# Optimization experiments

Hardware: AMD Instinct MI355X
Metric: run time of the kernel (lower is better)

The kernel has to match this reference:

```python
import jax, jax.numpy as jnp
import numpy as np
import math

CH, CTX, NH, G = 512, 768, 8, 32
EPS = 1e-5

def setup_inputs() -> dict:
    key = jax.random.key(0)
    ks = jax.random.split(key, 12)
    s = 0.02
    return {
        "x": jax.random.normal(ks[0], (1, CH, 64, 64), dtype=jnp.float32),
        "context": jax.random.normal(ks[1], (1, CTX, 64, 64), dtype=jnp.float32),
        "gn_w": jnp.ones((CH,), jnp.float32),
        "gn_b": jnp.zeros((CH,), jnp.float32),
        "wq": jax.random.normal(ks[2], (CH, CH), jnp.float32) * s,
        "bq": jnp.zeros((CH,), jnp.float32),
        "wk": jax.random.normal(ks[3], (CH, CTX), jnp.float32) * s,
        "bk": jnp.zeros((CH,), jnp.float32),
        "wv": jax.random.normal(ks[4], (CH, CTX), jnp.float32) * s,
        "bv": jnp.zeros((CH,), jnp.float32),
        "wo": jax.random.normal(ks[5], (CH, CH), jnp.float32) * s,
        "bo": jnp.zeros((CH,), jnp.float32),
    }

def _group_norm(x, w, b):
    B, C, H, W = x.shape
    r = x.reshape(B, G, C // G, H, W)
    mu = jnp.mean(r, axis=(2, 3, 4), keepdims=True)
    var = jnp.var(r, axis=(2, 3, 4), keepdims=True)
    r = (r - mu) * jax.lax.rsqrt(var + EPS)
    return r.reshape(B, C, H, W) * w[None, :, None, None] + b[None, :, None, None]

def _conv1x1(x, w, b):
    # x: [B,Cin,H,W], w: [Cout,Cin]
    return jnp.einsum('bchw,oc->bohw', x, w) + b[None, :, None, None]

def reference(x, context, gn_w, gn_b, wq, bq, wk, bk, wv, bv, wo, bo):
    B, C, H, W = x.shape
    residual = x
    h = _group_norm(x, gn_w, gn_b)
    q = _conv1x1(h, wq, bq).reshape(B, NH, C // NH, H * W)
    k = _conv1x1(context, wk, bk).reshape(B, NH, C // NH, H * W)
    v = _conv1x1(context, wv, bv).reshape(B, NH, C // NH, H * W)
    scale = 1.0 / math.sqrt(C // NH)
    # chunked softmax in the original is mathematically exact full softmax
    attn = jnp.einsum('bhdi,bhdj->bhij', q, k) * scale
    attn = jax.nn.softmax(attn, axis=-1)
    out = jnp.einsum('bhij,bhdj->bhdi', attn, v).reshape(B, C, H, W)
    out = _conv1x1(out, wo, bo)
    return out + residual
```

## Files before the change

kernel.cpp:

```cpp
#include <hip/hip_runtime.h>
#include <cstdint>
#include <cstddef>

typedef __attribute__((ext_vector_type(8))) short bf16x8;
typedef __attribute__((ext_vector_type(4))) float f32x4;
typedef unsigned short u16;

#define QSCALE (0.125f * 1.44269504088896f)

__device__ inline u16 f2bf(float x) {
  uint32_t u = __builtin_bit_cast(uint32_t, x);
  u += 0x7FFFu + ((u >> 16) & 1u);
  return (u16)(u >> 16);
}
__device__ inline float bf2f(u16 v) {
  return __builtin_bit_cast(float, (uint32_t)v << 16);
}
__device__ inline uint32_t cvtpk(float a, float b) {
  uint32_t r;
  asm("v_cvt_pk_bf16_f32 %0, %1, %2" : "=v"(r) : "v"(a), "v"(b));
  return r;
}
__device__ inline float exp2raw(float x) {
  float r;
  asm("v_exp_f32 %0, %1" : "=v"(r) : "v"(x));
  return r;
}
__device__ inline void gload_lds16(const void* g, void* l) {
  __builtin_amdgcn_global_load_lds(
      (const __attribute__((address_space(1))) char*)g,
      (__attribute__((address_space(3))) char*)l, 16, 0, 0);
}

__global__ __launch_bounds__(256) void gn_partial(const float* __restrict__ x,
                                                  float* __restrict__ gpart,
                                                  float* __restrict__ gpart2) {
  __shared__ float rs[4], rss[4];
  int b = blockIdx.x;
  int g = b >> 3, sl = b & 7;
  const float* base = x + (size_t)g * 65536 + sl * 8192;
  int t = threadIdx.x;
  float s = 0.f, ss = 0.f;
#pragma unroll
  for (int i = 0; i < 8; ++i) {
    float4 v = *reinterpret_cast<const float4*>(base + i * 1024 + t * 4);
    s += v.x + v.y + v.z + v.w;
    ss += v.x * v.x + v.y * v.y + v.z * v.z + v.w * v.w;
  }
  for (int d = 32; d; d >>= 1) {
    s += __shfl_down(s, d, 64);
    ss += __shfl_down(ss, d, 64);
  }
  int wid = t >> 6;
  if ((t & 63) == 0) { rs[wid] = s; rss[wid] = ss; }
  __syncthreads();
  if (t == 0) {
    gpart[b] = rs[0] + rs[1] + rs[2] + rs[3];
    gpart2[b] = rss[0] + rss[1] + rss[2] + rss[3];
  }
}

__global__ __launch_bounds__(256) void prep(const float* __restrict__ wq, u16* __restrict__ wqB,
                                            const float* __restrict__ wk, u16* __restrict__ wkB,
                                            const float* __restrict__ wv, u16* __restrict__ wvB,
                                            const float* __restrict__ wo, u16* __restrict__ woB,
                                            const float* __restrict__ x, u16* __restrict__ hT,
                                            const float* __restrict__ ctx, u16* __restrict__ ctxT,
                                            const float* __restrict__ gnw, const float* __restrict__ gnb,
                                            const float* __restrict__ gpart, const float* __restrict__ gpart2) {
  int b = blockIdx.x;
  int t = threadIdx.x;
  if (b < 1280) {
    const float* s; u16* d; int off;
    if (b < 256)       { s = wq; d = wqB; off = b; }
    else if (b < 640)  { s = wk; d = wkB; off = b - 256; }
    else if (b < 1024) { s = wv; d = wvB; off = b - 640; }
    else               { s = wo; d = woB; off = b - 1024; }
    int i = (off * 256 + t) * 4;
    float4 v = *reinterpret_cast<const float4*>(s + i);
    u16 o[4] = {f2bf(v.x), f2bf(v.y), f2bf(v.z), f2bf(v.w)};
    *reinterpret_cast<uint2*>(d + i) = *reinterpret_cast<const uint2*>(o);
    return;
  }
  __shared__ float tile[64][65];
  __shared__ float smu[4], srs[4];
  const float* in; u16* out; int C, p0, c0;
  bool norm = false;
  if (b < 1792) {
    int idx = b - 1280;
    in = x; out = hT; C = 512; p0 = (idx & 63) * 64; c0 = (idx >> 6) * 64; norm = true;
  } else {
    int idx = b - 1792;
    in = ctx; out = ctxT; C = 768; p0 = (idx & 63) * 64; c0 = (idx >> 6) * 64;
  }
  if (norm) {
    if (t < 4) {
      int g = (c0 >> 4) + t;
      float S = 0.f, SS = 0.f;
#pragma unroll
      for (int sIdx = 0; sIdx < 8; ++sIdx) {
        S += gpart[g * 8 + sIdx];
        SS += gpart2[g * 8 + sIdx];
      }
      float mu = S * (1.f / 65536.f);
      float var = SS * (1.f / 65536.f) - mu * mu;
      smu[t] = mu;
      srs[t] = rsqrtf(var + 1e-5f);
    }
    __syncthreads();
  }
  int cl = t >> 4, pl = (t & 15) * 4;
#pragma unroll
  for (int rep = 0; rep < 4; ++rep) {
    int c = cl + rep * 16;
    float4 v = *reinterpret_cast<const float4*>(in + (size_t)(c0 + c) * 4096 + p0 + pl);
    float s = 1.f, f = 0.f;
    if (norm) {
      s = gnw[c0 + c] * srs[rep];
      f = gnb[c0 + c] - smu[rep] * s;
    }
    tile[c][pl + 0] = v.x * s + f;
    tile[c][pl + 1] = v.y * s + f;
    tile[c][pl + 2] = v.z * s + f;
    tile[c][pl + 3] = v.w * s + f;
  }
  __syncthreads();
#pragma unroll
  for (int rep = 0; rep < 16; ++rep) {
    int idx = rep * 256 + t;
    int pw = idx >> 6, cw = idx & 63;
    out[(size_t)(p0 + pw) * C + c0 + cw] = f2bf(tile[cw][pw]);
  }
}

template <int BIAS_MODE>
__device__ inline void gemm_body(u16* __restrict__ aT, u16* __restrict__ bT,
                                 const u16* __restrict__ A, const u16* __restrict__ B,
                                 u16* __restrict__ Dv,
                                 const float* __restrict__ bias,
                                 int Rb, int K, float oscale, int bx, int by) {
  const int t = threadIdx.x;
  const int lane = t & 63, w = t >> 6;
  const int wr = w >> 1, wc = w & 1;
  const int l15 = lane & 15, l4 = lane >> 4;
  const int i0 = by * 128, j0 = bx * 64;
  const int r_st = t >> 3, slot = t & 7;
  f32x4 acc[4][2] = {};

  auto stage = [&](int kt, int b) {
#pragma unroll
    for (int q = 0; q < 4; ++q) {
      int row = q * 32 + r_st;
      int koff = kt + ((slot ^ (row & 7)) * 8);
      gload_lds16(A + (size_t)(i0 + row) * K + koff, (char*)aT + b * 16384 + q * 4096 + w * 1024);
    }
#pragma unroll
    for (int q = 0; q < 2; ++q) {
      int row = q * 32 + r_st;
      int koff = kt + ((slot ^ (row & 7)) * 8);
      gload_lds16(B + (size_t)(j0 + row) * K + koff, (char*)bT + b * 8192 + q * 4096 + w * 1024);
    }
  };

  const int nt = K / 64;
  stage(0, 0);
  stage(64, 1);

  for (int tt = 0; tt < nt; ++tt) {
    const int cur = tt % 3;
    if (tt + 1 < nt) asm volatile("s_waitcnt vmcnt(6)\n\ts_barrier" ::: "memory");
    else             asm volatile("s_waitcnt vmcnt(0)\n\ts_barrier" ::: "memory");
    if (tt + 2 < nt) stage((tt + 2) * 64, (tt + 2) % 3);

#pragma unroll
    for (int kk = 0; kk < 2; ++kk) {
      bf16x8 af[4], bfr[2];
#pragma unroll
      for (int m = 0; m < 4; ++m) {
        int row = wr * 64 + m * 16 + l15;
        int off = row * 128 + ((l4 * 16 + kk * 64) ^ ((row & 7) << 4));
        af[m] = *reinterpret_cast<const bf16x8*>((const char*)aT + cur * 16384 + off);
      }
#pragma unroll
      for (int n = 0; n < 2; ++n) {
        int row = wc * 32 + n * 16 + l15;
        int off = row * 128 + ((l4 * 16 + kk * 64) ^ ((row & 7) << 4));
        bfr[n] = *reinterpret_cast<const bf16x8*>((const char*)bT + cur * 8192 + off);
      }
#pragma unroll
      for (int m = 0; m < 4; ++m)
#pragma unroll
        for (int n = 0; n < 2; ++n)
          acc[m][n] = __builtin_amdgcn_mfma_f32_16x16x32_bf16(af[m], bfr[n], acc[m][n], 0, 0, 0);
    }
  }

#pragma unroll
  for (int m = 0; m < 4; ++m) {
    int ib = i0 + wr * 64 + m * 16 + l4 * 4;
#pragma unroll
    for (int n = 0; n < 2; ++n) {
      int j = j0 + wc * 32 + n * 16 + l15;
#pragma unroll
      for (int r = 0; r < 4; ++r) {
        int i = ib + r;
        float v = acc[m][n][r];
        if (BIAS_MODE == 0) v += bias[i];
        else v += bias[j];
        v *= oscale;
        Dv[(size_t)i * Rb + j] = f2bf(v);
      }
    }
  }
}

__global__ __launch_bounds__(256) void gemm_all(const u16* __restrict__ hT, const u16* __restrict__ ctxT,
                                                const u16* __restrict__ wqB, const u16* __restrict__ wkB,
                                                const u16* __restrict__ wvB,
                                                u16* __restrict__ QT, u16* __restrict__ KT, u16* __restrict__ Vb,
                                                const float* __restrict__ bq, const float* __restrict__ bk,
                                                const float* __restrict__ bv) {
  __shared__ u16 aT[3][128 * 64];
  __shared__ u16 bT[3][64 * 64];
  int b = blockIdx.x;
  if (b < 256)
    gemm_body<1>(&aT[0][0], &bT[0][0], hT, wqB, QT, bq, 512, 512, QSCALE, b & 7, b >> 3);
  else if (b < 512)
    gemm_body<1>(&aT[0][0], &bT[0][0], ctxT, wkB, KT, bk, 512, 768, 1.0f, (b - 256) & 7, (b - 256) >> 3);
  else
    gemm_body<0>(&aT[0][0], &bT[0][0], wvB, ctxT, Vb, bv, 4096, 768, 1.0f, (b - 512) & 63, (b - 512) >> 6);
}

__global__ __launch_bounds__(256) void gemm_projF(const u16* __restrict__ woB,
                                                  const u16* __restrict__ P0, const u16* __restrict__ P1,
                                                  const u16* __restrict__ P2, const u16* __restrict__ P3,
                                                  const float* __restrict__ Lb,
                                                  float* __restrict__ D, const float* __restrict__ bo,
                                                  const float* __restrict__ res) {
  __shared__ u16 aT[3][128 * 64];
  __shared__ u16 bT[2][64 * 64];
  __shared__ float sinv[512];
  const int t = threadIdx.x;
  const int lane = t & 63, w = t >> 6;
  const int wr = w >> 1, wc = w & 1;
  const int l15 = lane & 15, l4 = lane >> 4;
  const int bx = blockIdx.x & 63, by = blockIdx.x >> 6;
  const int i0 = by * 128, j0 = bx * 64;
  const int r_st = t >> 3, slot = t & 7;

  {
#pragma unroll
    for (int r = 0; r < 2; ++r) {
      int idx = t * 2 + r;
      int hh = idx >> 6, jj = idx & 63;
      int o = hh * 4096 + j0 + jj;
      float den = Lb[o] + Lb[32768 + o] + Lb[65536 + o] + Lb[98304 + o];
      sinv[idx] = 1.f / den;
    }
  }

  auto stageA = [&](int kt, int b) {
#pragma unroll
    for (int q = 0; q < 4; ++q) {
      int row = q * 32 + r_st;
      int koff = kt + ((slot ^ (row & 7)) * 8);
      gload_lds16(woB + (size_t)(i0 + row) * 512 + koff, (char*)aT + b * 16384 + q * 4096 + w * 1024);
    }
  };

  const int brow = t >> 2;
  const int bc0 = (t & 3) * 2;
  uint4 rv[2][4];
  auto loadB = [&](int kt) {
#pragma unroll
    for (int c = 0; c < 2; ++c) {
      size_t off = (size_t)(j0 + brow) * 512 + kt + (bc0 + c) * 8;
      rv[c][0] = *reinterpret_cast<const uint4*>(P0 + off);
      rv[c][1] = *reinterpret_cast<const uint4*>(P1 + off);
      rv[c][2] = *reinterpret_cast<const uint4*>(P2 + off);
      rv[c][3] = *reinterpret_cast<const uint4*>(P3 + off);
    }
  };
  auto writeB = [&](int kt, int buf) {
    float inv = sinv[((kt >> 6) << 6) + brow];
#pragma unroll
    for (int c = 0; c < 2; ++c) {
      uint32_t pk[4];
#pragma unroll
      for (int wi = 0; wi < 4; ++wi) {
        uint32_t w0 = (wi == 0) ? rv[c][0].x : (wi == 1) ? rv[c][0].y : (wi == 2) ? rv[c][0].z : rv[c][0].w;
        uint32_t w1 = (wi == 0) ? rv[c][1].x : (wi == 1) ? rv[c][1].y : (wi == 2) ? rv[c][1].z : rv[c][1].w;
        uint32_t w2 = (wi == 0) ? rv[c][2].x : (wi == 1) ? rv[c][2].y : (wi == 2) ? rv[c][2].z : rv[c][2].w;
        uint32_t w3 = (wi == 0) ? rv[c][3].x : (wi == 1) ? rv[c][3].y : (wi == 2) ? rv[c][3].z : rv[c][3].w;
        float lo = __builtin_bit_cast(float, w0 << 16) + __builtin_bit_cast(float, w1 << 16) +
                   __builtin_bit_cast(float, w2 << 16) + __builtin_bit_cast(float, w3 << 16);
        float hi = __builtin_bit_cast(float, w0 & 0xFFFF0000u) + __builtin_bit_cast(float, w1 & 0xFFFF0000u) +
                   __builtin_bit_cast(float, w2 & 0xFFFF0000u) + __builtin_bit_cast(float, w3 & 0xFFFF0000u);
        pk[wi] = cvtpk(lo * inv, hi * inv);
      }
      uint4 outv = {pk[0], pk[1], pk[2], pk[3]};
      int off = brow * 128 + (((bc0 + c) ^ (brow & 7)) * 16);
      *reinterpret_cast<uint4*>((char*)&bT[buf][0] + off) = outv;
    }
  };

  stageA(0, 0);
  stageA(64, 1);
  loadB(0);
  asm volatile("s_waitcnt vmcnt(4)" ::: "memory");
  writeB(0, 0);
  asm volatile("s_waitcnt lgkmcnt(0)\n\ts_barrier" ::: "memory");

  f32x4 acc[4][2] = {};
  for (int tt = 0; tt < 8; ++tt) {
    const int cur = tt & 1;
    if (tt + 1 < 8) loadB((tt + 1) * 64);

#pragma unroll
    for (int kk = 0; kk < 2; ++kk) {
      bf16x8 af[4], bfr[2];
#pragma unroll
      for (int m = 0; m < 4; ++m) {
        int row = wr * 64 + m * 16 + l15;
        int off = row * 128 + ((l4 * 16 + kk * 64) ^ ((row & 7) << 4));
        af[m] = *reinterpret_cast<const bf16x8*>((const char*)aT + (tt % 3) * 16384 + off);
      }
#pragma unroll
      for (int n = 0; n < 2; ++n) {
        int row = wc * 32 + n * 16 + l15;
        int off = row * 128 + ((l4 * 16 + kk * 64) ^ ((row & 7) << 4));
        bfr[n] = *reinterpret_cast<const bf16x8*>((const char*)&bT[cur][0] + off);
      }
#pragma unroll
      for (int m = 0; m < 4; ++m)
#pragma unroll
        for (int n = 0; n < 2; ++n)
          acc[m][n] = __builtin_amdgcn_mfma_f32_16x16x32_bf16(af[m], bfr[n], acc[m][n], 0, 0, 0);
    }

    if (tt + 2 < 8) stageA((tt + 2) * 64, (tt + 2) % 3);
    if (tt + 1 < 8) {
      if (tt + 2 < 8) asm volatile("s_waitcnt vmcnt(4)" ::: "memory");
      else            asm volatile("s_waitcnt vmcnt(0)" ::: "memory");
      writeB((tt + 1) * 64, cur ^ 1);
    }
    asm volatile("s_waitcnt lgkmcnt(0)\n\ts_barrier" ::: "memory");
  }

#pragma unroll
  for (int m = 0; m < 4; ++m) {
    int ib = i0 + wr * 64 + m * 16 + l4 * 4;
#pragma unroll
    for (int n = 0; n < 2; ++n) {
      int j = j0 + wc * 32 + n * 16 + l15;
#pragma unroll
      for (int r = 0; r < 4; ++r) {
        int i = ib + r;
        float v = acc[m][n][r] + bo[i] + res[(size_t)i * 4096 + j];
        D[(size_t)i * 4096 + j] = v;
      }
    }
  }
}

__global__ __launch_bounds__(256) void attn_kernel(const u16* __restrict__ QT,
                                                   const u16* __restrict__ KT,
                                                   const u16* __restrict__ V,
                                                   u16* __restrict__ P0, u16* __restrict__ P1,
                                                   u16* __restrict__ P2, u16* __restrict__ P3,
                                                   float* __restrict__ Lb) {
  __shared__ u16 kbuf[2][64 * 64];
  __shared__ u16 vbuf[2][64 * 64];
  const int t = threadIdx.x;
  const int lane = t & 63, w = t >> 6;
  const int l15 = lane & 15, l4 = lane >> 4;
  int id = blockIdx.x;
  id = (id & 7) * 128 + (id >> 3);
  const int z = id >> 8;
  const int h = (id >> 5) & 7;
  const int q0 = (id & 31) * 128;
  const int tile0 = z * 16;
  const int r_st = t >> 3, slot = t & 7;

  bf16x8 qa[2][2];
#pragma unroll
  for (int f = 0; f < 2; ++f) {
    int qrow = q0 + w * 32 + f * 16 + l15;
    qa[f][0] = *reinterpret_cast<const bf16x8*>(QT + (size_t)qrow * 512 + h * 64 + l4 * 8);
    qa[f][1] = *reinterpret_cast<const bf16x8*>(QT + (size_t)qrow * 512 + h * 64 + 32 + l4 * 8);
  }

  f32x4 o0[4] = {}, o1[4] = {};
  f32x4 la0 = {}, la1 = {};
  const short oneb = (short)0x3F80;
  const bf16x8 ones = {oneb, oneb, oneb, oneb, oneb, oneb, oneb, oneb};

  int off0[4], off1[4];
#pragma unroll
  for (int n = 0; n < 4; ++n) {
    int row = n * 16 + l15, sw = (row & 7) << 4;
    off0[n] = row * 128 + ((l4 * 16) ^ sw);
    off1[n] = row * 128 + ((l4 * 16 + 64) ^ sw);
  }

  auto stageK = [&](int tile, int b) {
#pragma unroll
    for (int q = 0; q < 2; ++q) {
      int row = q * 32 + r_st;
      int so = (slot ^ (row & 7)) * 8;
      gload_lds16(KT + (size_t)(tile * 64 + row) * 512 + h * 64 + so,
                  (char*)kbuf[b] + q * 4096 + w * 1024);
    }
  };
  auto stageV = [&](int tile, int b) {
#pragma unroll
    for (int q = 0; q < 2; ++q) {
      int row = q * 32 + r_st;
      int so = ((((slot & 1) * 4 + (slot >> 1)) ^ (row & 7)) * 8);
      gload_lds16(V + (size_t)(h * 64 + row) * 4096 + tile * 64 + so,
                  (char*)vbuf[b] + q * 4096 + w * 1024);
    }
  };

  stageK(tile0, 0);
  stageV(tile0, 0);

#pragma unroll 2
  for (int kt = 0; kt < 16; ++kt) {
    const int cur = kt & 1;
    asm volatile("s_waitcnt vmcnt(0)\n\ts_barrier" ::: "memory");
    if (kt + 1 < 16) { stageK(tile0 + kt + 1, cur ^ 1); stageV(tile0 + kt + 1, cur ^ 1); }

    f32x4 s0[4], s1[4];
#pragma unroll
    for (int n = 0; n < 4; ++n) {
      bf16x8 kb0 = *reinterpret_cast<const bf16x8*>((const char*)kbuf[cur] + off0[n]);
      bf16x8 kb1 = *reinterpret_cast<const bf16x8*>((const char*)kbuf[cur] + off1[n]);
      f32x4 za = {};
      za = __builtin_amdgcn_mfma_f32_16x16x32_bf16(kb0, qa[0][0], za, 0, 0, 0);
      za = __builtin_amdgcn_mfma_f32_16x16x32_bf16(kb1, qa[0][1], za, 0, 0, 0);
      s0[n] = za;
      f32x4 zb = {};
      zb = __builtin_amdgcn_mfma_f32_16x16x32_bf16(kb0, qa[1][0], zb, 0, 0, 0);
      zb = __builtin_amdgcn_mfma_f32_16x16x32_bf16(kb1, qa[1][1], zb, 0, 0, 0);
      s1[n] = zb;
    }

#pragma unroll
    for (int n = 0; n < 4; ++n)
#pragma unroll
      for (int r = 0; r < 4; ++r) {
        s0[n][r] = exp2raw(s0[n][r]);
        s1[n][r] = exp2raw(s1[n][r]);
      }

    bf16x8 pa[2][2];
    {
      uint32_t u00 = cvtpk(s0[0][0], s0[0][1]), u01 = cvtpk(s0[0][2], s0[0][3]);
      uint32_t u10 = cvtpk(s0[1][0], s0[1][1]), u11 = cvtpk(s0[1][2], s0[1][3]);
      uint32_t u20 = cvtpk(s0[2][0], s0[2][1]), u21 = cvtpk(s0[2][2], s0[2][3]);
      uint32_t u30 = cvtpk(s0[3][0], s0[3][1]), u31 = cvtpk(s0[3][2], s0[3][3]);
      asm volatile("v_permlane16_swap_b32 %0, %1" : "+v"(u00), "+v"(u20));
      asm volatile("v_permlane16_swap_b32 %0, %1" : "+v"(u01), "+v"(u21));
      asm volatile("v_permlane16_swap_b32 %0, %1" : "+v"(u10), "+v"(u30));
      asm volatile("v_permlane16_swap_b32 %0, %1" : "+v"(u11), "+v"(u31));
      int4 p0i = {(int)u00, (int)u01, (int)u20, (int)u21};
      int4 p1i = {(int)u10, (int)u11, (int)u30, (int)u31};
      pa[0][0] = __builtin_bit_cast(bf16x8, p0i);
      pa[0][1] = __builtin_bit_cast(bf16x8, p1i);
    }
    {
      uint32_t u00 = cvtpk(s1[0][0], s1[0][1]), u01 = cvtpk(s1[0][2], s1[0][3]);
      uint32_t u10 = cvtpk(s1[1][0], s1[1][1]), u11 = cvtpk(s1[1][2], s1[1][3]);
      uint32_t u20 = cvtpk(s1[2][0], s1[2][1]), u21 = cvtpk(s1[2][2], s1[2][3]);
      uint32_t u30 = cvtpk(s1[3][0], s1[3][1]), u31 = cvtpk(s1[3][2], s1[3][3]);
      asm volatile("v_permlane16_swap_b32 %0, %1" : "+v"(u00), "+v"(u20));
      asm volatile("v_permlane16_swap_b32 %0, %1" : "+v"(u01), "+v"(u21));
      asm volatile("v_permlane16_swap_b32 %0, %1" : "+v"(u10), "+v"(u30));
      asm volatile("v_permlane16_swap_b32 %0, %1" : "+v"(u11), "+v"(u31));
      int4 p0i = {(int)u00, (int)u01, (int)u20, (int)u21};
      int4 p1i = {(int)u10, (int)u11, (int)u30, (int)u31};
      pa[1][0] = __builtin_bit_cast(bf16x8, p0i);
      pa[1][1] = __builtin_bit_cast(bf16x8, p1i);
    }

    la0 = __builtin_amdgcn_mfma_f32_16x16x32_bf16(pa[0][0], ones, la0, 0, 0, 0);
    la0 = __builtin_amdgcn_mfma_f32_16x16x32_bf16(pa[0][1], ones, la0, 0, 0, 0);
    la1 = __builtin_amdgcn_mfma_f32_16x16x32_bf16(pa[1][0], ones, la1, 0, 0, 0);
    la1 = __builtin_amdgcn_mfma_f32_16x16x32_bf16(pa[1][1], ones, la1, 0, 0, 0);

#pragma unroll
    for (int dt = 0; dt < 4; ++dt) {
      bf16x8 vb0 = *reinterpret_cast<const bf16x8*>((const char*)vbuf[cur] + off0[dt]);
      bf16x8 vb1 = *reinterpret_cast<const bf16x8*>((const char*)vbuf[cur] + off1[dt]);
      o0[dt] = __builtin_amdgcn_mfma_f32_16x16x32_bf16(pa[0][0], vb0, o0[dt], 0, 0, 0);
      o0[dt] = __builtin_amdgcn_mfma_f32_16x16x32_bf16(pa[0][1], vb1, o0[dt], 0, 0, 0);
      o1[dt] = __builtin_amdgcn_mfma_f32_16x16x32_bf16(pa[1][0], vb0, o1[dt], 0, 0, 0);
      o1[dt] = __builtin_amdgcn_mfma_f32_16x16x32_bf16(pa[1][1], vb1, o1[dt], 0, 0, 0);
    }
  }

  u16* obase = (z == 0) ? P0 : (z == 1) ? P1 : (z == 2) ? P2 : P3;
#pragma unroll
  for (int r = 0; r < 4; ++r) {
    int orow0 = q0 + w * 32 + l4 * 4 + r;
#pragma unroll
    for (int dt = 0; dt < 4; ++dt) {
      obase[(size_t)orow0 * 512 + h * 64 + dt * 16 + l15] = f2bf(o0[dt][r]);
      obase[(size_t)(orow0 + 16) * 512 + h * 64 + dt * 16 + l15] = f2bf(o1[dt][r]);
    }
  }
  if (l15 == 0) {
    int q = q0 + w * 32 + l4 * 4;
#pragma unroll
    for (int r = 0; r < 4; ++r) {
      Lb[z * 32768 + h * 4096 + q + r] = la0[r];
      Lb[z * 32768 + h * 4096 + q + r + 16] = la1[r];
    }
  }
}

extern "C" void kernel_launch(void* const* d_in, const int* in_sizes, int n_in,
                              void* d_out, int out_size, void* d_ws, size_t ws_size,
                              hipStream_t stream) {
  const float* x    = (const float*)d_in[0];
  const float* ctx  = (const float*)d_in[1];
  const float* gn_w = (const float*)d_in[2];
  const float* gn_b = (const float*)d_in[3];
  const float* wq   = (const float*)d_in[4];
  const float* bq   = (const float*)d_in[5];
  const float* wk   = (const float*)d_in[6];
  const float* bk   = (const float*)d_in[7];
  const float* wv   = (const float*)d_in[8];
  const float* bv   = (const float*)d_in[9];
  const float* wo   = (const float*)d_in[10];
  const float* bo   = (const float*)d_in[11];

  char* ws = (char*)d_ws;
  float* gpart  = (float*)ws;
  float* gpart2 = gpart + 256;
  u16* woB    = (u16*)(ws + 4096);
  u16* wqB    = woB + 512 * 512;
  u16* wkB    = wqB + 512 * 512;
  u16* wvB    = wkB + 512 * 768;
  u16* hT     = wvB + 512 * 768;
  u16* ctxT   = hT + 4096 * 512;
  u16* QT     = ctxT + 4096 * 768;
  u16* KT     = QT + 4096 * 512;
  u16* Vb     = KT + 4096 * 512;
  u16* OtT    = Vb + (size_t)512 * 4096;
  float* Lb   = (float*)(OtT + (size_t)4096 * 512);
  u16* P0     = wqB;
  u16* P1     = P0 + (size_t)4096 * 512;
  u16* P2     = P1 + (size_t)4096 * 512;
  u16* P3     = OtT;

  gn_partial<<<256, 256, 0, stream>>>(x, gpart, gpart2);
  prep<<<2560, 256, 0, stream>>>(wq, wqB, wk, wkB, wv, wvB, wo, woB,
                                 x, hT, ctx, ctxT, gn_w, gn_b, gpart, gpart2);

  gemm_all<<<768, 256, 0, stream>>>(hT, ctxT, wqB, wkB, wvB, QT, KT, Vb, bq, bk, bv);

  attn_kernel<<<1024, 256, 0, stream>>>(QT, KT, Vb, P0, P1, P2, P3, Lb);

  gemm_projF<<<256, 256, 0, stream>>>(woB, P0, P1, P2, P3, Lb, (float*)d_out, bo, x);
}
```

Baseline: 96.47 us.

## Regroup prep kernels to overlap stats with casts; double-buffer QKV GEMM

Merges the group-norm partial-statistics pass with the weight casts and the context transpose into one launch. The normalize-and-transpose of x moves into a second kernel, so only that part waits on the statistics and the independent work overlaps with the reduction. Separately, the QKV GEMM goes from triple buffering (two stages of prefetch) to double buffering with a full vmcnt(0) wait each step. That cuts LDS use and may raise occupancy, at the cost of less latency hiding for global loads.

```diff
diff --git a/kernel.cpp b/kernel.cpp
--- a/kernel.cpp
+++ b/kernel.cpp
@@ -32,50 +32,47 @@
       (__attribute__((address_space(3))) char*)l, 16, 0, 0);
 }
 
-__global__ __launch_bounds__(256) void gn_partial(const float* __restrict__ x,
-                                                  float* __restrict__ gpart,
-                                                  float* __restrict__ gpart2) {
-  __shared__ float rs[4], rss[4];
-  int b = blockIdx.x;
-  int g = b >> 3, sl = b & 7;
-  const float* base = x + (size_t)g * 65536 + sl * 8192;
-  int t = threadIdx.x;
-  float s = 0.f, ss = 0.f;
-#pragma unroll
-  for (int i = 0; i < 8; ++i) {
-    float4 v = *reinterpret_cast<const float4*>(base + i * 1024 + t * 4);
-    s += v.x + v.y + v.z + v.w;
-    ss += v.x * v.x + v.y * v.y + v.z * v.z + v.w * v.w;
-  }
-  for (int d = 32; d; d >>= 1) {
-    s += __shfl_down(s, d, 64);
-    ss += __shfl_down(ss, d, 64);
-  }
-  int wid = t >> 6;
-  if ((t & 63) == 0) { rs[wid] = s; rss[wid] = ss; }
-  __syncthreads();
-  if (t == 0) {
-    gpart[b] = rs[0] + rs[1] + rs[2] + rs[3];
-    gpart2[b] = rss[0] + rss[1] + rss[2] + rss[3];
-  }
-}
-
-__global__ __launch_bounds__(256) void prep(const float* __restrict__ wq, u16* __restrict__ wqB,
-                                            const float* __restrict__ wk, u16* __restrict__ wkB,
-                                            const float* __restrict__ wv, u16* __restrict__ wvB,
-                                            const float* __restrict__ wo, u16* __restrict__ woB,
-                                            const float* __restrict__ x, u16* __restrict__ hT,
-                                            const float* __restrict__ ctx, u16* __restrict__ ctxT,
-                                            const float* __restrict__ gnw, const float* __restrict__ gnb,
-                                            const float* __restrict__ gpart, const float* __restrict__ gpart2) {
+__global__ __launch_bounds__(256) void prep_a(const float* __restrict__ x,
+                                              float* __restrict__ gpart,
+                                              float* __restrict__ gpart2,
+                                              const float* __restrict__ wq, u16* __restrict__ wqB,
+                                              const float* __restrict__ wk, u16* __restrict__ wkB,
+                                              const float* __restrict__ wv, u16* __restrict__ wvB,
+                                              const float* __restrict__ wo, u16* __restrict__ woB,
+                                              const float* __restrict__ ctx, u16* __restrict__ ctxT) {
   int b = blockIdx.x;
   int t = threadIdx.x;
-  if (b < 1280) {
-    const float* s; u16* d; int off;
-    if (b < 256)       { s = wq; d = wqB; off = b; }
-    else if (b < 640)  { s = wk; d = wkB; off = b - 256; }
-    else if (b < 1024) { s = wv; d = wvB; off = b - 640; }
-    else               { s = wo; d = woB; off = b - 1024; }
+  if (b < 256) {
+    __shared__ float rs[4], rss[4];
+    int g = b >> 3, sl = b & 7;
+    const float* base = x + (size_t)g * 65536 + sl * 8192;
+    float s = 0.f, ss = 0.f;
+#pragma unroll
+    for (int i = 0; i < 8; ++i) {
+      float4 v = *reinterpret_cast<const float4*>(base + i * 1024 + t * 4);
+      s += v.x + v.y + v.z + v.w;
+      ss += v.x * v.x + v.y * v.y + v.z * v.z + v.w * v.w;
+    }
+    for (int d = 32; d; d >>= 1) {
+      s += __shfl_down(s, d, 64);
+      ss += __shfl_down(ss, d, 64);
+    }
+    int wid = t >> 6;
+    if ((t & 63) == 0) { rs[wid] = s; rss[wid] = ss; }
+    __syncthreads();
+    if (t == 0) {
+      gpart[b] = rs[0] + rs[1] + rs[2] + rs[3];
+      gpart2[b] = rss[0] + rss[1] + rss[2] + rss[3];
+    }
+    return;
+  }
+  if (b < 1536) {
+    int off = b - 256;
+    const float* s; u16* d;
+    if (off < 256)       { s = wq; d = wqB; }
+    else if (off < 640)  { s = wk; d = wkB; off -= 256; }
+    else if (off < 1024) { s = wv; d = wvB; off -= 640; }
+    else                 { s = wo; d = woB; off -= 1024; }
     int i = (off * 256 + t) * 4;
     float4 v = *reinterpret_cast<const float4*>(s + i);
     u16 o[4] = {f2bf(v.x), f2bf(v.y), f2bf(v.z), f2bf(v.w)};
@@ -83,42 +80,57 @@
     return;
   }
   __shared__ float tile[64][65];
-  __shared__ float smu[4], srs[4];
-  const float* in; u16* out; int C, p0, c0;
-  bool norm = false;
-  if (b < 1792) {
-    int idx = b - 1280;
-    in = x; out = hT; C = 512; p0 = (idx & 63) * 64; c0 = (idx >> 6) * 64; norm = true;
-  } else {
-    int idx = b - 1792;
-    in = ctx; out = ctxT; C = 768; p0 = (idx & 63) * 64; c0 = (idx >> 6) * 64;
-  }
-  if (norm) {
-    if (t < 4) {
-      int g = (c0 >> 4) + t;
-      float S = 0.f, SS = 0.f;
-#pragma unroll
-      for (int sIdx = 0; sIdx < 8; ++sIdx) {
-        S += gpart[g * 8 + sIdx];
-        SS += gpart2[g * 8 + sIdx];
-      }
-      float mu = S * (1.f / 65536.f);
-      float var = SS * (1.f / 65536.f) - mu * mu;
-      smu[t] = mu;
-      srs[t] = rsqrtf(var + 1e-5f);
-    }
-    __syncthreads();
-  }
+  int idx = b - 1536;
+  int p0 = (idx & 63) * 64, c0 = (idx >> 6) * 64;
   int cl = t >> 4, pl = (t & 15) * 4;
 #pragma unroll
   for (int rep = 0; rep < 4; ++rep) {
     int c = cl + rep * 16;
-    float4 v = *reinterpret_cast<const float4*>(in + (size_t)(c0 + c) * 4096 + p0 + pl);
-    float s = 1.f, f = 0.f;
-    if (norm) {
-      s = gnw[c0 + c] * srs[rep];
-      f = gnb[c0 + c] - smu[rep] * s;
-    }
+    float4 v = *reinterpret_cast<const float4*>(ctx + (size_t)(c0 + c) * 4096 + p0 + pl);
+    tile[c][pl + 0] = v.x;
+    tile[c][pl + 1] = v.y;
+    tile[c][pl + 2] = v.z;
+    tile[c][pl + 3] = v.w;
+  }
+  __syncthreads();
+#pragma unroll
+  for (int rep = 0; rep < 16; ++rep) {
+    int id2 = rep * 256 + t;
+    int pw = id2 >> 6, cw = id2 & 63;
+    ctxT[(size_t)(p0 + pw) * 768 + c0 + cw] = f2bf(tile[cw][pw]);
+  }
+}
+
+__global__ __launch_bounds__(256) void prep_b(const float* __restrict__ x,
+                                              u16* __restrict__ hT,
+                                              const float* __restrict__ gnw, const float* __restrict__ gnb,
+                                              const float* __restrict__ gpart, const float* __restrict__ gpart2) {
+  __shared__ float tile[64][65];
+  __shared__ float smu[4], srs[4];
+  int b = blockIdx.x;
+  int t = threadIdx.x;
+  int p0 = (b & 63) * 64, c0 = (b >> 6) * 64;
+  if (t < 4) {
+    int g = (c0 >> 4) + t;
+    float S = 0.f, SS = 0.f;
+#pragma unroll
+    for (int sIdx = 0; sIdx < 8; ++sIdx) {
+      S += gpart[g * 8 + sIdx];
+      SS += gpart2[g * 8 + sIdx];
+    }
+    float mu = S * (1.f / 65536.f);
+    float var = SS * (1.f / 65536.f) - mu * mu;
+    smu[t] = mu;
+    srs[t] = rsqrtf(var + 1e-5f);
+  }
+  __syncthreads();
+  int cl = t >> 4, pl = (t & 15) * 4;
+#pragma unroll
+  for (int rep = 0; rep < 4; ++rep) {
+    int c = cl + rep * 16;
+    float4 v = *reinterpret_cast<const float4*>(x + (size_t)(c0 + c) * 4096 + p0 + pl);
+    float s = gnw[c0 + c] * srs[rep];
+    float f = gnb[c0 + c] - smu[rep] * s;
     tile[c][pl + 0] = v.x * s + f;
     tile[c][pl + 1] = v.y * s + f;
     tile[c][pl + 2] = v.z * s + f;
@@ -129,7 +141,7 @@
   for (int rep = 0; rep < 16; ++rep) {
     int idx = rep * 256 + t;
     int pw = idx >> 6, cw = idx & 63;
-    out[(size_t)(p0 + pw) * C + c0 + cw] = f2bf(tile[cw][pw]);
+    hT[(size_t)(p0 + pw) * 512 + c0 + cw] = f2bf(tile[cw][pw]);
   }
 }
 
@@ -164,13 +176,11 @@
 
   const int nt = K / 64;
   stage(0, 0);
-  stage(64, 1);
 
   for (int tt = 0; tt < nt; ++tt) {
-    const int cur = tt % 3;
-    if (tt + 1 < nt) asm volatile("s_waitcnt vmcnt(6)\n\ts_barrier" ::: "memory");
-    else             asm volatile("s_waitcnt vmcnt(0)\n\ts_barrier" ::: "memory");
-    if (tt + 2 < nt) stage((tt + 2) * 64, (tt + 2) % 3);
+    const int cur = tt & 1;
+    asm volatile("s_waitcnt vmcnt(0)\n\ts_barrier" ::: "memory");
+    if (tt + 1 < nt) stage((tt + 1) * 64, cur ^ 1);
 
 #pragma unroll
     for (int kk = 0; kk < 2; ++kk) {
@@ -220,8 +230,8 @@
                                                 u16* __restrict__ QT, u16* __restrict__ KT, u16* __restrict__ Vb,
                                                 const float* __restrict__ bq, const float* __restrict__ bk,
                                                 const float* __restrict__ bv) {
-  __shared__ u16 aT[3][128 * 64];
-  __shared__ u16 bT[3][64 * 64];
+  __shared__ u16 aT[2][128 * 64];
+  __shared__ u16 bT[2][64 * 64];
   int b = blockIdx.x;
   if (b < 256)
     gemm_body<1>(&aT[0][0], &bT[0][0], hT, wqB, QT, bq, 512, 512, QSCALE, b & 7, b >> 3);
@@ -555,9 +565,8 @@
   u16* P2     = P1 + (size_t)4096 * 512;
   u16* P3     = OtT;
 
-  gn_partial<<<256, 256, 0, stream>>>(x, gpart, gpart2);
-  prep<<<2560, 256, 0, stream>>>(wq, wqB, wk, wkB, wv, wvB, wo, woB,
-                                 x, hT, ctx, ctxT, gn_w, gn_b, gpart, gpart2);
+  prep_a<<<2304, 256, 0, stream>>>(x, gpart, gpart2, wq, wqB, wk, wkB, wv, wvB, wo, woB, ctx, ctxT);
+  prep_b<<<512, 256, 0, stream>>>(x, hT, gn_w, gn_b, gpart, gpart2);
 
   gemm_all<<<768, 256, 0, stream>>>(hT, ctxT, wqB, wkB, wvB, QT, KT, Vb, bq, bk, bv);
 
```

Measured after the change: 92.19 us (median of 3 runs). 4.4% less time.
